# Kernel tuning notes

Measured on AMD Instinct MI355X. Metric: run time of the kernel, lower is better.

Reference implementation:

```python
import jax, jax.numpy as jnp
import numpy as np

N_NODES = 50000
EMBED_DIM = 128
N_EDGES = 600000
ALPHA = 0.2  # LeakyReLU negative slope


def setup_inputs() -> dict:
    key = jax.random.key(0)
    k1, k2 = jax.random.split(key)
    drug_embeddings = jax.random.normal(k1, (N_NODES, EMBED_DIM), dtype=jnp.float32)
    drug_relationships = jax.random.randint(k2, (N_EDGES, 2), 0, N_NODES, dtype=jnp.int64)
    return {"drug_embeddings": drug_embeddings, "drug_relationships": drug_relationships}


def reference(drug_embeddings, drug_relationships):
    # edge_index = drug_relationships.T : row 0 = target/source node i, row 1 = neighbor j
    src = drug_relationships[:, 0]  # [E]
    dst = drug_relationships[:, 1]  # [E]
    drug_i = drug_embeddings[src]   # [E, D] gather
    drug_j = drug_embeddings[dst]   # [E, D] gather
    # per-edge dot-product score with LeakyReLU
    scores = jax.nn.leaky_relu(jnp.sum(drug_i * drug_j, axis=1), negative_slope=ALPHA)  # [E]
    # NOTE: original applies a single GLOBAL softmax over all edges (dim=0), not per-node
    att = jax.nn.softmax(scores, axis=0)  # [E]
    weighted = drug_j * att[:, None]      # [E, D]
    # scatter_add back onto source nodes
    h_prime = jax.ops.segment_sum(weighted, src, num_segments=drug_embeddings.shape[0])  # [N, D]
    return h_prime + drug_embeddings
```

## Files before the change

### kernel.cpp

```cpp
#include <hip/hip_runtime.h>
#include <hip/hip_fp16.h>
#include <math.h>

constexpr int kNodes = 50000;
constexpr int kEdges = 600000;
constexpr float kAlpha = 0.2f;
constexpr float kNegBig = -1e30f;

constexpr int kCap = 40;

constexpr int kNodeBlocks = kNodes / 8;
constexpr int kEdgeBlocks = (kEdges + 255) / 256;

constexpr int kOffCounts = 16;
constexpr int kOffCsr    = kOffCounts + kNodes;
constexpr int kOffPart   = kOffCsr + kNodes * kCap;
constexpr int kOffMnode  = kOffPart + 2 * kNodeBlocks;
constexpr int kOffH      = kOffMnode + kNodes;
constexpr int kEndH      = kOffH + kNodes * 64;

__device__ __forceinline__ void onlineMerge(float& m, float& s, float m2, float s2) {
    const float M = fmaxf(m, m2);
    s = s * __expf(m - M) + s2 * __expf(m2 - M);
    m = M;
}

__global__ __launch_bounds__(256)
void conv_kernel(const float4* __restrict__ emb4, uint2* __restrict__ hTab) {
    const int i = blockIdx.x * 256 + threadIdx.x;
    const float4 v = emb4[i];
    const __half2 h0 = __floats2half2_rn(v.x, v.y);
    const __half2 h1 = __floats2half2_rn(v.z, v.w);
    uint2 r;
    __builtin_memcpy(&r.x, &h0, 4);
    __builtin_memcpy(&r.y, &h1, 4);
    hTab[i] = r;
}

__global__ __launch_bounds__(256)
void build_kernel(const int2* __restrict__ rel2,
                  int* __restrict__ counts,
                  int* __restrict__ csr) {
    const int e = blockIdx.x * 256 + threadIdx.x;
    if (e < kEdges) {
        const int2 sd = rel2[e];
        const int pos = atomicAdd(&counts[sd.x], 1);
        if (pos < kCap)
            csr[sd.x * kCap + pos] = sd.y;
    }
}

template <bool F16>
__global__ __launch_bounds__(256)
void scores_kernel(const float4* __restrict__ emb4,
                   const uint2*  __restrict__ hTab,
                   const int*    __restrict__ counts,
                   const int*    __restrict__ csr,
                   float4* __restrict__ out4,
                   float*  __restrict__ mnode,
                   float2* __restrict__ partials) {
    const int tid = threadIdx.x;
    const int g   = tid & 31;
    const int grp = tid >> 5;
    const int node = blockIdx.x * 8 + grp;

    const float4 a = emb4[(unsigned)node * 32u + g];
    const int cnt = min(counts[node], kCap);
    unsigned int lo = 0, hi = 0;
    if (2 * g < cnt) {
        const int2 pr = *(const int2*)(csr + node * kCap + 2 * g);
        lo = (unsigned int)pr.x; hi = (unsigned int)pr.y;
    }

    float4 acc = make_float4(0.f, 0.f, 0.f, 0.f);
    float m_run = kNegBig, s_run = 0.0f;

    auto loadB = [&](int d) -> float4 {
        if constexpr (F16) {
            const uint2 r = hTab[(unsigned)d * 32u + g];
            __half2 h0, h1;
            __builtin_memcpy(&h0, &r.x, 4);
            __builtin_memcpy(&h1, &r.y, 4);
            const float2 f0 = __half22float2(h0);
            const float2 f1 = __half22float2(h1);
            return make_float4(f0.x, f0.y, f1.x, f1.y);
        } else {
            return emb4[(unsigned)d * 32u + g];
        }
    };

    int k = 0;
    for (; k + 3 < cnt; k += 4) {
        const int h = k >> 1;
        const int d0 = (int)__shfl(lo, h, 32);
        const int d1 = (int)__shfl(hi, h, 32);
        const int d2 = (int)__shfl(lo, h + 1, 32);
        const int d3 = (int)__shfl(hi, h + 1, 32);
        const float4 b0 = loadB(d0);
        const float4 b1 = loadB(d1);
        const float4 b2 = loadB(d2);
        const float4 b3 = loadB(d3);
        float p0 = a.x*b0.x + a.y*b0.y + a.z*b0.z + a.w*b0.w;
        float p1 = a.x*b1.x + a.y*b1.y + a.z*b1.z + a.w*b1.w;
        float p2 = a.x*b2.x + a.y*b2.y + a.z*b2.z + a.w*b2.w;
        float p3 = a.x*b3.x + a.y*b3.y + a.z*b3.z + a.w*b3.w;
        #pragma unroll
        for (int o = 16; o > 0; o >>= 1) {
            p0 += __shfl_xor(p0, o); p1 += __shfl_xor(p1, o);
            p2 += __shfl_xor(p2, o); p3 += __shfl_xor(p3, o);
        }
        const float s0 = p0 > 0.f ? p0 : kAlpha * p0;
        const float s1 = p1 > 0.f ? p1 : kAlpha * p1;
        const float s2 = p2 > 0.f ? p2 : kAlpha * p2;
        const float s3 = p3 > 0.f ? p3 : kAlpha * p3;
        const float m4 = fmaxf(fmaxf(s0, s1), fmaxf(s2, s3));
        if (m4 > m_run) {
            const float rs = __expf(m_run - m4);
            s_run *= rs;
            acc.x *= rs; acc.y *= rs; acc.z *= rs; acc.w *= rs;
            m_run = m4;
        }
        const float w0e = __expf(s0 - m_run);
        const float w1e = __expf(s1 - m_run);
        const float w2e = __expf(s2 - m_run);
        const float w3e = __expf(s3 - m_run);
        s_run += w0e + w1e + w2e + w3e;
        acc.x += w0e*b0.x + w1e*b1.x + w2e*b2.x + w3e*b3.x;
        acc.y += w0e*b0.y + w1e*b1.y + w2e*b2.y + w3e*b3.y;
        acc.z += w0e*b0.z + w1e*b1.z + w2e*b2.z + w3e*b3.z;
        acc.w += w0e*b0.w + w1e*b1.w + w2e*b2.w + w3e*b3.w;
    }
    for (; k < cnt; ++k) {
        const unsigned int wv = (k & 1) ? hi : lo;
        const int d0 = (int)__shfl(wv, k >> 1, 32);
        const float4 b0 = loadB(d0);
        float p0 = a.x*b0.x + a.y*b0.y + a.z*b0.z + a.w*b0.w;
        #pragma unroll
        for (int o = 16; o > 0; o >>= 1) p0 += __shfl_xor(p0, o);
        const float s0 = p0 > 0.f ? p0 : kAlpha * p0;
        if (s0 > m_run) {
            const float rs = __expf(m_run - s0);
            s_run *= rs;
            acc.x *= rs; acc.y *= rs; acc.z *= rs; acc.w *= rs;
            m_run = s0;
        }
        const float w0e = __expf(s0 - m_run);
        s_run += w0e;
        acc.x += w0e*b0.x; acc.y += w0e*b0.y; acc.z += w0e*b0.z; acc.w += w0e*b0.w;
    }

    out4[(unsigned)node * 32u + g] = acc;
    if (g == 0) mnode[node] = m_run;

    __shared__ float sm[8];
    __shared__ float ss[8];
    if (g == 0) { sm[grp] = m_run; ss[grp] = s_run; }
    __syncthreads();
    if (tid == 0) {
        float M = sm[0], S = ss[0];
        #pragma unroll
        for (int i = 1; i < 8; ++i) onlineMerge(M, S, sm[i], ss[i]);
        partials[blockIdx.x] = make_float2(M, S);
    }
}

__global__ __launch_bounds__(1024)
void final_kernel(const float2* __restrict__ partials, float* __restrict__ wsf) {
    float M = kNegBig, S = 0.0f;
    for (int i = threadIdx.x; i < kNodeBlocks; i += 1024) {
        const float2 p = partials[i];
        onlineMerge(M, S, p.x, p.y);
    }
    __shared__ float fm[1024];
    __shared__ float fs[1024];
    fm[threadIdx.x] = M; fs[threadIdx.x] = S;
    __syncthreads();
    for (int s = 512; s > 0; s >>= 1) {
        if ((int)threadIdx.x < s) {
            float m1 = fm[threadIdx.x], s1 = fs[threadIdx.x];
            onlineMerge(m1, s1, fm[threadIdx.x + s], fs[threadIdx.x + s]);
            fm[threadIdx.x] = m1; fs[threadIdx.x] = s1;
        }
        __syncthreads();
    }
    if (threadIdx.x == 0) { wsf[0] = fm[0]; wsf[1] = 1.0f / fs[0]; }
}

__global__ __launch_bounds__(256)
void epi_kernel(const float4* __restrict__ emb4,
                const float*  __restrict__ mnode,
                const float*  __restrict__ wsf,
                float4* __restrict__ out4) {
    const int i = blockIdx.x * 256 + threadIdx.x;
    const int node = i >> 5;
    const float scale = __expf(mnode[node] - wsf[0]) * wsf[1];
    const float4 o = out4[i];
    const float4 e = emb4[i];
    out4[i] = make_float4(e.x + scale * o.x, e.y + scale * o.y,
                          e.z + scale * o.z, e.w + scale * o.w);
}

extern "C" void kernel_launch(void* const* d_in, const int* in_sizes, int n_in,
                              void* d_out, int out_size, void* d_ws, size_t ws_size,
                              hipStream_t stream) {
    const float4* emb4 = (const float4*)d_in[0];
    const int2*   rel2 = (const int2*)d_in[1];
    float4* out4 = (float4*)d_out;
    float*  wsf  = (float*)d_ws;
    int*    wsi  = (int*)d_ws;

    int*    counts   = wsi + kOffCounts;
    int*    csr      = wsi + kOffCsr;
    float2* partials = (float2*)(wsi + kOffPart);
    float*  mnode    = wsf + kOffMnode;
    uint2*  hTab     = (uint2*)(wsi + kOffH);

    const bool f16 = ws_size >= (size_t)kEndH * sizeof(int);

    hipMemsetAsync(counts, 0, (size_t)kNodes * sizeof(int), stream);
    if (f16)
        hipLaunchKernelGGL(conv_kernel, dim3(kNodeBlocks), dim3(256), 0, stream, emb4, hTab);
    hipLaunchKernelGGL(build_kernel, dim3(kEdgeBlocks), dim3(256), 0, stream, rel2, counts, csr);
    if (f16)
        hipLaunchKernelGGL((scores_kernel<true>), dim3(kNodeBlocks), dim3(256), 0, stream,
                           emb4, hTab, counts, csr, out4, mnode, partials);
    else
        hipLaunchKernelGGL((scores_kernel<false>), dim3(kNodeBlocks), dim3(256), 0, stream,
                           emb4, hTab, counts, csr, out4, mnode, partials);
    hipLaunchKernelGGL(final_kernel, dim3(1), dim3(1024), 0, stream, partials, wsf);
    hipLaunchKernelGGL(epi_kernel, dim3(kNodeBlocks), dim3(256), 0, stream,
                       emb4, mnode, wsf, out4);
}
```

Baseline: 166.6 us.

## Fuse prep kernels and fold global softmax reduction into last scores block

Merges the fp16 conversion and CSR build kernels into one launch with block-range dispatch. It also removes the separate single-block final reduction kernel. The last scores block, found through an atomic completion counter, now merges all per-block partials. This cuts two kernel launches and their inter-kernel gaps, but adds an atomic handshake and a serial tail reduction on one 256-thread block. Memory ordering relies on relaxed atomics plus a vmcnt wait, with no acquire on the reader side.

```diff
diff --git a/kernel.cpp b/kernel.cpp
--- a/kernel.cpp
+++ b/kernel.cpp
@@ -12,6 +12,7 @@
 constexpr int kNodeBlocks = kNodes / 8;
 constexpr int kEdgeBlocks = (kEdges + 255) / 256;
 
+constexpr int kOffDone   = 8;
 constexpr int kOffCounts = 16;
 constexpr int kOffCsr    = kOffCounts + kNodes;
 constexpr int kOffPart   = kOffCsr + kNodes * kCap;
@@ -25,28 +26,31 @@
     m = M;
 }
 
+template <bool F16>
 __global__ __launch_bounds__(256)
-void conv_kernel(const float4* __restrict__ emb4, uint2* __restrict__ hTab) {
-    const int i = blockIdx.x * 256 + threadIdx.x;
-    const float4 v = emb4[i];
-    const __half2 h0 = __floats2half2_rn(v.x, v.y);
-    const __half2 h1 = __floats2half2_rn(v.z, v.w);
-    uint2 r;
-    __builtin_memcpy(&r.x, &h0, 4);
-    __builtin_memcpy(&r.y, &h1, 4);
-    hTab[i] = r;
-}
-
-__global__ __launch_bounds__(256)
-void build_kernel(const int2* __restrict__ rel2,
-                  int* __restrict__ counts,
-                  int* __restrict__ csr) {
-    const int e = blockIdx.x * 256 + threadIdx.x;
-    if (e < kEdges) {
-        const int2 sd = rel2[e];
-        const int pos = atomicAdd(&counts[sd.x], 1);
-        if (pos < kCap)
-            csr[sd.x * kCap + pos] = sd.y;
+void prep_kernel(const float4* __restrict__ emb4,
+                 const int2*  __restrict__ rel2,
+                 uint2* __restrict__ hTab,
+                 int* __restrict__ counts,
+                 int* __restrict__ csr) {
+    constexpr int convBlocks = F16 ? kNodeBlocks : 0;
+    if (F16 && (int)blockIdx.x < convBlocks) {
+        const int i = blockIdx.x * 256 + threadIdx.x;
+        const float4 v = emb4[i];
+        const __half2 h0 = __floats2half2_rn(v.x, v.y);
+        const __half2 h1 = __floats2half2_rn(v.z, v.w);
+        uint2 r;
+        __builtin_memcpy(&r.x, &h0, 4);
+        __builtin_memcpy(&r.y, &h1, 4);
+        hTab[i] = r;
+    } else {
+        const int e = ((int)blockIdx.x - convBlocks) * 256 + (int)threadIdx.x;
+        if (e < kEdges) {
+            const int2 sd = rel2[e];
+            const int pos = atomicAdd(&counts[sd.x], 1);
+            if (pos < kCap)
+                csr[sd.x * kCap + pos] = sd.y;
+        }
     }
 }
 
@@ -58,7 +62,10 @@
                    const int*    __restrict__ csr,
                    float4* __restrict__ out4,
                    float*  __restrict__ mnode,
-                   float2* __restrict__ partials) {
+                   float*  __restrict__ wsf) {
+    int* wsi = (int*)wsf;
+    unsigned long long* part64 = (unsigned long long*)(wsi + kOffPart);
+
     const int tid = threadIdx.x;
     const int g   = tid & 31;
     const int grp = tid >> 5;
@@ -154,36 +161,46 @@
 
     __shared__ float sm[8];
     __shared__ float ss[8];
+    __shared__ int  isLast;
     if (g == 0) { sm[grp] = m_run; ss[grp] = s_run; }
     __syncthreads();
     if (tid == 0) {
         float M = sm[0], S = ss[0];
         #pragma unroll
         for (int i = 1; i < 8; ++i) onlineMerge(M, S, sm[i], ss[i]);
-        partials[blockIdx.x] = make_float2(M, S);
-    }
-}
-
-__global__ __launch_bounds__(1024)
-void final_kernel(const float2* __restrict__ partials, float* __restrict__ wsf) {
-    float M = kNegBig, S = 0.0f;
-    for (int i = threadIdx.x; i < kNodeBlocks; i += 1024) {
-        const float2 p = partials[i];
-        onlineMerge(M, S, p.x, p.y);
-    }
-    __shared__ float fm[1024];
-    __shared__ float fs[1024];
-    fm[threadIdx.x] = M; fs[threadIdx.x] = S;
+        float2 p = make_float2(M, S);
+        unsigned long long bits;
+        __builtin_memcpy(&bits, &p, 8);
+        __hip_atomic_store(part64 + blockIdx.x, bits,
+                           __ATOMIC_RELAXED, __HIP_MEMORY_SCOPE_AGENT);
+        asm volatile("s_waitcnt vmcnt(0)" ::: "memory");
+        const int old = __hip_atomic_fetch_add(wsi + kOffDone, 1,
+                                               __ATOMIC_RELAXED, __HIP_MEMORY_SCOPE_AGENT);
+        isLast = (old == kNodeBlocks - 1);
+    }
     __syncthreads();
-    for (int s = 512; s > 0; s >>= 1) {
-        if ((int)threadIdx.x < s) {
-            float m1 = fm[threadIdx.x], s1 = fs[threadIdx.x];
-            onlineMerge(m1, s1, fm[threadIdx.x + s], fs[threadIdx.x + s]);
-            fm[threadIdx.x] = m1; fs[threadIdx.x] = s1;
-        }
+
+    if (isLast) {
+        float M = kNegBig, S = 0.0f;
+        const float2* pp = (const float2*)(wsi + kOffPart);
+        for (int i = tid; i < kNodeBlocks; i += 256) {
+            const float2 p = pp[i];
+            onlineMerge(M, S, p.x, p.y);
+        }
+        __shared__ float fm[256];
+        __shared__ float fs[256];
+        fm[tid] = M; fs[tid] = S;
         __syncthreads();
-    }
-    if (threadIdx.x == 0) { wsf[0] = fm[0]; wsf[1] = 1.0f / fs[0]; }
+        for (int s = 128; s > 0; s >>= 1) {
+            if (tid < s) {
+                float m1 = fm[tid], s1 = fs[tid];
+                onlineMerge(m1, s1, fm[tid + s], fs[tid + s]);
+                fm[tid] = m1; fs[tid] = s1;
+            }
+            __syncthreads();
+        }
+        if (tid == 0) { wsf[0] = fm[0]; wsf[1] = 1.0f / fs[0]; }
+    }
 }
 
 __global__ __launch_bounds__(256)
@@ -209,25 +226,26 @@
     float*  wsf  = (float*)d_ws;
     int*    wsi  = (int*)d_ws;
 
-    int*    counts   = wsi + kOffCounts;
-    int*    csr      = wsi + kOffCsr;
-    float2* partials = (float2*)(wsi + kOffPart);
-    float*  mnode    = wsf + kOffMnode;
-    uint2*  hTab     = (uint2*)(wsi + kOffH);
+    int*    counts = wsi + kOffCounts;
+    int*    csr    = wsi + kOffCsr;
+    float*  mnode  = wsf + kOffMnode;
+    uint2*  hTab   = (uint2*)(wsi + kOffH);
 
     const bool f16 = ws_size >= (size_t)kEndH * sizeof(int);
 
-    hipMemsetAsync(counts, 0, (size_t)kNodes * sizeof(int), stream);
-    if (f16)
-        hipLaunchKernelGGL(conv_kernel, dim3(kNodeBlocks), dim3(256), 0, stream, emb4, hTab);
-    hipLaunchKernelGGL(build_kernel, dim3(kEdgeBlocks), dim3(256), 0, stream, rel2, counts, csr);
-    if (f16)
+    hipMemsetAsync(wsi + kOffDone, 0,
+                   (size_t)(kOffCounts + kNodes - kOffDone) * sizeof(int), stream);
+    if (f16) {
+        hipLaunchKernelGGL((prep_kernel<true>), dim3(kNodeBlocks + kEdgeBlocks), dim3(256),
+                           0, stream, emb4, rel2, hTab, counts, csr);
         hipLaunchKernelGGL((scores_kernel<true>), dim3(kNodeBlocks), dim3(256), 0, stream,
-                           emb4, hTab, counts, csr, out4, mnode, partials);
-    else
+                           emb4, hTab, counts, csr, out4, mnode, wsf);
+    } else {
+        hipLaunchKernelGGL((prep_kernel<false>), dim3(kEdgeBlocks), dim3(256),
+                           0, stream, emb4, rel2, hTab, counts, csr);
         hipLaunchKernelGGL((scores_kernel<false>), dim3(kNodeBlocks), dim3(256), 0, stream,
-                           emb4, hTab, counts, csr, out4, mnode, partials);
-    hipLaunchKernelGGL(final_kernel, dim3(1), dim3(1024), 0, stream, partials, wsf);
+                           emb4, hTab, counts, csr, out4, mnode, wsf);
+    }
     hipLaunchKernelGGL(epi_kernel, dim3(kNodeBlocks), dim3(256), 0, stream,
                        emb4, mnode, wsf, out4);
 }
```

Measured after the change: 221.7 us. 1.33x slower.

## Replace global softmax reduction kernel with double atomic sum and fuse memset

Applied to the files above, without the earlier changes.

Drops the single-block final reduction kernel. Each scores block now accumulates sum(s*exp(m)) directly into a double-precision global scalar with atomicAdd. The epilogue computes exp(m_node)/S in double. Zeroing of counts and the accumulator moves into the conversion kernel, which removes the memset launch. The cost is 6250 contended double atomics and unshifted exponentials in double, which could overflow or lose accuracy if scores were very large.

```diff
diff --git a/kernel.cpp b/kernel.cpp
--- a/kernel.cpp
+++ b/kernel.cpp
@@ -14,8 +14,7 @@
 
 constexpr int kOffCounts = 16;
 constexpr int kOffCsr    = kOffCounts + kNodes;
-constexpr int kOffPart   = kOffCsr + kNodes * kCap;
-constexpr int kOffMnode  = kOffPart + 2 * kNodeBlocks;
+constexpr int kOffMnode  = kOffCsr + kNodes * kCap;
 constexpr int kOffH      = kOffMnode + kNodes;
 constexpr int kEndH      = kOffH + kNodes * 64;
 
@@ -26,7 +25,10 @@
 }
 
 __global__ __launch_bounds__(256)
-void conv_kernel(const float4* __restrict__ emb4, uint2* __restrict__ hTab) {
+void conv_kernel(const float4* __restrict__ emb4,
+                 uint2* __restrict__ hTab,
+                 int* __restrict__ counts,
+                 double* __restrict__ s0) {
     const int i = blockIdx.x * 256 + threadIdx.x;
     const float4 v = emb4[i];
     const __half2 h0 = __floats2half2_rn(v.x, v.y);
@@ -35,6 +37,8 @@
     __builtin_memcpy(&r.x, &h0, 4);
     __builtin_memcpy(&r.y, &h1, 4);
     hTab[i] = r;
+    if (i < kNodes) counts[i] = 0;
+    if (i == 0) *s0 = 0.0;
 }
 
 __global__ __launch_bounds__(256)
@@ -58,7 +62,7 @@
                    const int*    __restrict__ csr,
                    float4* __restrict__ out4,
                    float*  __restrict__ mnode,
-                   float2* __restrict__ partials) {
+                   double* __restrict__ s0) {
     const int tid = threadIdx.x;
     const int g   = tid & 31;
     const int grp = tid >> 5;
@@ -109,21 +113,21 @@
             p0 += __shfl_xor(p0, o); p1 += __shfl_xor(p1, o);
             p2 += __shfl_xor(p2, o); p3 += __shfl_xor(p3, o);
         }
-        const float s0 = p0 > 0.f ? p0 : kAlpha * p0;
-        const float s1 = p1 > 0.f ? p1 : kAlpha * p1;
-        const float s2 = p2 > 0.f ? p2 : kAlpha * p2;
-        const float s3 = p3 > 0.f ? p3 : kAlpha * p3;
-        const float m4 = fmaxf(fmaxf(s0, s1), fmaxf(s2, s3));
+        const float s0f = p0 > 0.f ? p0 : kAlpha * p0;
+        const float s1f = p1 > 0.f ? p1 : kAlpha * p1;
+        const float s2f = p2 > 0.f ? p2 : kAlpha * p2;
+        const float s3f = p3 > 0.f ? p3 : kAlpha * p3;
+        const float m4 = fmaxf(fmaxf(s0f, s1f), fmaxf(s2f, s3f));
         if (m4 > m_run) {
             const float rs = __expf(m_run - m4);
             s_run *= rs;
             acc.x *= rs; acc.y *= rs; acc.z *= rs; acc.w *= rs;
             m_run = m4;
         }
-        const float w0e = __expf(s0 - m_run);
-        const float w1e = __expf(s1 - m_run);
-        const float w2e = __expf(s2 - m_run);
-        const float w3e = __expf(s3 - m_run);
+        const float w0e = __expf(s0f - m_run);
+        const float w1e = __expf(s1f - m_run);
+        const float w2e = __expf(s2f - m_run);
+        const float w3e = __expf(s3f - m_run);
         s_run += w0e + w1e + w2e + w3e;
         acc.x += w0e*b0.x + w1e*b1.x + w2e*b2.x + w3e*b3.x;
         acc.y += w0e*b0.y + w1e*b1.y + w2e*b2.y + w3e*b3.y;
@@ -137,14 +141,14 @@
         float p0 = a.x*b0.x + a.y*b0.y + a.z*b0.z + a.w*b0.w;
         #pragma unroll
         for (int o = 16; o > 0; o >>= 1) p0 += __shfl_xor(p0, o);
-        const float s0 = p0 > 0.f ? p0 : kAlpha * p0;
-        if (s0 > m_run) {
-            const float rs = __expf(m_run - s0);
+        const float s0f = p0 > 0.f ? p0 : kAlpha * p0;
+        if (s0f > m_run) {
+            const float rs = __expf(m_run - s0f);
             s_run *= rs;
             acc.x *= rs; acc.y *= rs; acc.z *= rs; acc.w *= rs;
-            m_run = s0;
-        }
-        const float w0e = __expf(s0 - m_run);
+            m_run = s0f;
+        }
+        const float w0e = __expf(s0f - m_run);
         s_run += w0e;
         acc.x += w0e*b0.x; acc.y += w0e*b0.y; acc.z += w0e*b0.z; acc.w += w0e*b0.w;
     }
@@ -157,43 +161,23 @@
     if (g == 0) { sm[grp] = m_run; ss[grp] = s_run; }
     __syncthreads();
     if (tid == 0) {
-        float M = sm[0], S = ss[0];
+        double t = 0.0;
         #pragma unroll
-        for (int i = 1; i < 8; ++i) onlineMerge(M, S, sm[i], ss[i]);
-        partials[blockIdx.x] = make_float2(M, S);
-    }
-}
-
-__global__ __launch_bounds__(1024)
-void final_kernel(const float2* __restrict__ partials, float* __restrict__ wsf) {
-    float M = kNegBig, S = 0.0f;
-    for (int i = threadIdx.x; i < kNodeBlocks; i += 1024) {
-        const float2 p = partials[i];
-        onlineMerge(M, S, p.x, p.y);
-    }
-    __shared__ float fm[1024];
-    __shared__ float fs[1024];
-    fm[threadIdx.x] = M; fs[threadIdx.x] = S;
-    __syncthreads();
-    for (int s = 512; s > 0; s >>= 1) {
-        if ((int)threadIdx.x < s) {
-            float m1 = fm[threadIdx.x], s1 = fs[threadIdx.x];
-            onlineMerge(m1, s1, fm[threadIdx.x + s], fs[threadIdx.x + s]);
-            fm[threadIdx.x] = m1; fs[threadIdx.x] = s1;
-        }
-        __syncthreads();
-    }
-    if (threadIdx.x == 0) { wsf[0] = fm[0]; wsf[1] = 1.0f / fs[0]; }
+        for (int i = 0; i < 8; ++i)
+            t += (double)ss[i] * exp((double)sm[i]);
+        atomicAdd(s0, t);
+    }
 }
 
 __global__ __launch_bounds__(256)
 void epi_kernel(const float4* __restrict__ emb4,
                 const float*  __restrict__ mnode,
-                const float*  __restrict__ wsf,
+                const double* __restrict__ s0,
                 float4* __restrict__ out4) {
     const int i = blockIdx.x * 256 + threadIdx.x;
     const int node = i >> 5;
-    const float scale = __expf(mnode[node] - wsf[0]) * wsf[1];
+    const double S = *s0;
+    const float scale = (float)(exp((double)mnode[node]) / S);
     const float4 o = out4[i];
     const float4 e = emb4[i];
     out4[i] = make_float4(e.x + scale * o.x, e.y + scale * o.y,
@@ -209,25 +193,28 @@
     float*  wsf  = (float*)d_ws;
     int*    wsi  = (int*)d_ws;
 
-    int*    counts   = wsi + kOffCounts;
-    int*    csr      = wsi + kOffCsr;
-    float2* partials = (float2*)(wsi + kOffPart);
-    float*  mnode    = wsf + kOffMnode;
-    uint2*  hTab     = (uint2*)(wsi + kOffH);
+    double* s0     = (double*)d_ws;
+    int*    counts = wsi + kOffCounts;
+    int*    csr    = wsi + kOffCsr;
+    float*  mnode  = wsf + kOffMnode;
+    uint2*  hTab   = (uint2*)(wsi + kOffH);
 
     const bool f16 = ws_size >= (size_t)kEndH * sizeof(int);
 
-    hipMemsetAsync(counts, 0, (size_t)kNodes * sizeof(int), stream);
-    if (f16)
-        hipLaunchKernelGGL(conv_kernel, dim3(kNodeBlocks), dim3(256), 0, stream, emb4, hTab);
-    hipLaunchKernelGGL(build_kernel, dim3(kEdgeBlocks), dim3(256), 0, stream, rel2, counts, csr);
-    if (f16)
+    if (f16) {
+        hipLaunchKernelGGL(conv_kernel, dim3(kNodeBlocks), dim3(256), 0, stream,
+                           emb4, hTab, counts, s0);
+        hipLaunchKernelGGL(build_kernel, dim3(kEdgeBlocks), dim3(256), 0, stream,
+                           rel2, counts, csr);
         hipLaunchKernelGGL((scores_kernel<true>), dim3(kNodeBlocks), dim3(256), 0, stream,
-                           emb4, hTab, counts, csr, out4, mnode, partials);
-    else
+                           emb4, hTab, counts, csr, out4, mnode, s0);
+    } else {
+        hipMemsetAsync(d_ws, 0, (size_t)kOffCsr * sizeof(int), stream);
+        hipLaunchKernelGGL(build_kernel, dim3(kEdgeBlocks), dim3(256), 0, stream,
+                           rel2, counts, csr);
         hipLaunchKernelGGL((scores_kernel<false>), dim3(kNodeBlocks), dim3(256), 0, stream,
-                           emb4, hTab, counts, csr, out4, mnode, partials);
-    hipLaunchKernelGGL(final_kernel, dim3(1), dim3(1024), 0, stream, partials, wsf);
+                           emb4, hTab, counts, csr, out4, mnode, s0);
+    }
     hipLaunchKernelGGL(epi_kernel, dim3(kNodeBlocks), dim3(256), 0, stream,
-                       emb4, mnode, wsf, out4);
-}
+                       emb4, mnode, s0, out4);
+}
```

New measurement: 210.1 us. +26.2%, slower.
